# Kernel optimization log

Measured on AMD Instinct MI355X. Metric: run time of the kernel, lower is better.

## Reference

```python
import jax, jax.numpy as jnp
import numpy as np

HDIM = 1024
N_CLASSES = 50257
CUTOFFS = [2000, 10000, N_CLASSES]  # shortlist=2000, clusters: [2000,10000), [10000,50257)
DIV = 4.0
HEAD_SIZE = CUTOFFS[0] + 2  # shortlist + 2 cluster logits


def setup_inputs() -> dict:
    key = jax.random.key(0)
    ks = jax.random.split(key, 12)
    B, S, K = 8, 512, 256
    N = B * K
    hsz0 = int(HDIM // (DIV ** 1))  # 256
    hsz1 = int(HDIM // (DIV ** 2))  # 64
    osz0 = CUTOFFS[1] - CUTOFFS[0]  # 8000
    osz1 = CUTOFFS[2] - CUTOFFS[1]  # 40257
    w = 0.02
    return {
        "targets": jax.random.randint(ks[0], (N,), 0, N_CLASSES),
        "last_hidden_states": jax.random.normal(ks[1], (B, S, HDIM), dtype=jnp.float32),
        "cls_tokens_batch": jax.random.normal(ks[2], (B, HDIM), dtype=jnp.float32),
        "idx": jax.random.randint(ks[3], (B, K), 0, S),
        "head_W": jax.random.normal(ks[4], (HEAD_SIZE, HDIM), dtype=jnp.float32) * w,
        "head_b": jnp.zeros((HEAD_SIZE,), dtype=jnp.float32),
        "proj0_W": jax.random.normal(ks[5], (hsz0, HDIM), dtype=jnp.float32) * w,
        "out0_W": jax.random.normal(ks[6], (osz0, hsz0), dtype=jnp.float32) * w,
        "proj1_W": jax.random.normal(ks[7], (hsz1, HDIM), dtype=jnp.float32) * w,
        "out1_W": jax.random.normal(ks[8], (osz1, hsz1), dtype=jnp.float32) * w,
    }


def reference(targets, last_hidden_states, cls_tokens_batch, idx,
              head_W, head_b, proj0_W, out0_W, proj1_W, out1_W):
    # Gather context token embeddings: [B, K, H] -> [N, H]
    B, S, H = last_hidden_states.shape
    x = last_hidden_states[jnp.arange(B)[:, None], idx].reshape(-1, H)
    N = x.shape[0]
    c0, c1 = CUTOFFS[0], CUTOFFS[1]

    # Head: shortlist logits + per-cluster routing logits, [N, c0+2]
    head_logprob = jax.nn.log_softmax(x @ head_W.T + head_b, axis=-1)
    # Tail clusters: low-rank projection then output GEMM + log-softmax
    lp0 = jax.nn.log_softmax((x @ proj0_W.T) @ out0_W.T, axis=-1)  # [N, 8000]
    lp1 = jax.nn.log_softmax((x @ proj1_W.T) @ out1_W.T, axis=-1)  # [N, 40257]

    n = jnp.arange(N)
    t = targets
    short = head_logprob[n, jnp.clip(t, 0, c0 - 1)]
    mid = head_logprob[:, c0] + lp0[n, jnp.clip(t - c0, 0, lp0.shape[1] - 1)]
    high = head_logprob[:, c0 + 1] + lp1[n, jnp.clip(t - c1, 0, lp1.shape[1] - 1)]
    out = jnp.where(t < c0, short, jnp.where(t < c1, mid, high))  # target log-probs [N]
    loss = -jnp.mean(out)
    return out, loss
```

## Files before the change

kernel.cpp:

```cpp
#include <hip/hip_runtime.h>
#include <hip/hip_bf16.h>

#define NROWS 2048
#define L2E 1.4426950408889634f

typedef float f32x4 __attribute__((ext_vector_type(4)));
typedef __bf16 bf16x8 __attribute__((ext_vector_type(8)));
typedef short s16x8 __attribute__((ext_vector_type(8)));

typedef const __attribute__((address_space(1))) unsigned int* gas_t;
typedef __attribute__((address_space(3))) unsigned int* las_t;

__device__ __forceinline__ unsigned short f2bf(float f) {
    unsigned int u = __float_as_uint(f);
    unsigned int r = (u + 0x7FFFu + ((u >> 16) & 1u)) >> 16;
    return (unsigned short)r;
}
__device__ __forceinline__ float bf2f(unsigned short u) {
    return __uint_as_float((unsigned int)u << 16);
}
__device__ __forceinline__ f32x4 mfma16(s16x8 a, s16x8 b, f32x4 c) {
    return __builtin_amdgcn_mfma_f32_16x16x32_bf16(
        __builtin_bit_cast(bf16x8, a), __builtin_bit_cast(bf16x8, b), c, 0, 0, 0);
}

__global__ void k_prologue(const float* __restrict__ lhs, const int* __restrict__ idx,
                           const float* __restrict__ hw, const float* __restrict__ p0w,
                           const float* __restrict__ p1w, const float* __restrict__ hb,
                           const int* __restrict__ tgt,
                           unsigned short* __restrict__ xb, unsigned short* __restrict__ hWb,
                           unsigned short* __restrict__ pW01,
                           float* __restrict__ bias_s, int* __restrict__ tc,
                           unsigned long long* __restrict__ lossacc,
                           unsigned int* __restrict__ ticket) {
    int bid = blockIdx.x;
    if (bid < 2048) {
        int tid = bid * 256 + threadIdx.x;
        int n = tid >> 8;
        int c = (tid & 255) << 2;
        int b = n >> 8, k = n & 255;
        int srow = idx[(b << 8) + k];
        const float4 v = *reinterpret_cast<const float4*>(
            lhs + (((size_t)b << 9) + srow) * 1024 + c);
        ushort4 o = make_ushort4(f2bf(v.x), f2bf(v.y), f2bf(v.z), f2bf(v.w));
        *reinterpret_cast<ushort4*>(xb + (size_t)n * 1024 + c) = o;
        return;
    }
    bid -= 2048;
    if (bid < 2432) {
        long e = ((long)bid * 256 + threadIdx.x) * 4;
        const long B0 = 2048L * 1024;
        if (e < B0) {
            float4 v = *reinterpret_cast<const float4*>(hw + e);
            long row = e >> 10;
            ushort4 o;
            if (row < 2002) {
                o = make_ushort4(f2bf(v.x * L2E), f2bf(v.y * L2E), f2bf(v.z * L2E), f2bf(v.w * L2E));
            } else {
                o = make_ushort4(0, 0, 0, 0);
            }
            *reinterpret_cast<ushort4*>(hWb + e) = o;
        } else {
            long l = e - B0;
            long row = l >> 10;
            ushort4 o;
            if (row < 256) {
                float4 v = *reinterpret_cast<const float4*>(p0w + l);
                o = make_ushort4(f2bf(v.x), f2bf(v.y), f2bf(v.z), f2bf(v.w));
            } else if (row < 320) {
                float4 v = *reinterpret_cast<const float4*>(p1w + (l - 256L * 1024));
                o = make_ushort4(f2bf(v.x), f2bf(v.y), f2bf(v.z), f2bf(v.w));
            } else {
                o = make_ushort4(0, 0, 0, 0);
            }
            *reinterpret_cast<ushort4*>(pW01 + l) = o;
        }
        return;
    }
    bid -= 2432;
    int n = bid * 256 + threadIdx.x;
    if (n >= 2048) return;
    if (n == 0) { *lossacc = 0ull; *ticket = 0u; }
    bias_s[n] = (n < 2002) ? hb[n] * L2E : -1e30f;
    int t = tgt[n];
    tc[n] = min(t, 1999);
    tc[2048 + n] = min(max(t - 2000, 0), 7999);
    tc[4096 + n] = min(max(t - 10000, 0), 40256);
}

#define CVT_Y0 19
template <int NT>
__global__ __launch_bounds__(256)
void k_mid(const unsigned short* __restrict__ A, int lda,
           const unsigned short* __restrict__ B, int ldb,
           const float* __restrict__ bias, float* __restrict__ partial,
           unsigned short* __restrict__ hout, int hstride, int hcols, int fsplit,
           const float* __restrict__ o0w, const float* __restrict__ o1w,
           unsigned short* __restrict__ o0Wb, unsigned short* __restrict__ o1Wb) {
    if ((int)blockIdx.y >= CVT_Y0) {
        const long E0 = 8064L * 256;
        const long E1 = E0 + 40320L * 64;
        long cb = (long)(blockIdx.y - CVT_Y0) * 32 + blockIdx.x;
        long e = (cb * 256 + threadIdx.x) * 4;
        if (e >= E1) return;
        const float* src; unsigned short* dst; long rows; int colshift;
        if (e < E0) { src = o0w; dst = o0Wb; rows = 8000;  colshift = 8; }
        else        { e -= E0; src = o1w; dst = o1Wb; rows = 40257; colshift = 6; }
        long row = e >> colshift;
        ushort4 o;
        if (row < rows) {
            float4 v = *reinterpret_cast<const float4*>(src + e);
            o = make_ushort4(f2bf(v.x * L2E), f2bf(v.y * L2E), f2bf(v.z * L2E), f2bf(v.w * L2E));
        } else {
            o = make_ushort4(0, 0, 0, 0);
        }
        *reinterpret_cast<ushort4*>(dst + e) = o;
        return;
    }
    __shared__ unsigned short As[2][64 * 64];
    __shared__ unsigned short Bs[2][128 * 64];
    const int tid = threadIdx.x;
    const int lane = tid & 63, wid = tid >> 6;
    const int wc = wid;
    const int g = lane >> 4, cl = lane & 15;
    const int row0 = blockIdx.x * 64;
    const int col0 = blockIdx.y * 128;

    const int sr = wid * 8 + (lane >> 3);
    const int swz = ((lane & 7) ^ (lane >> 3)) * 8;
    const unsigned short* Ab = A + (size_t)(row0 + sr) * lda + swz;
    const unsigned short* Bb = B + (size_t)(col0 + sr) * ldb + swz;

    auto stage = [&](int buf, int kt) {
        unsigned short* la = &As[buf][wid * 8 * 64];
        unsigned short* lb = &Bs[buf][wid * 8 * 64];
#pragma unroll
        for (int i = 0; i < 2; ++i)
            __builtin_amdgcn_global_load_lds((gas_t)(const void*)(Ab + kt + (size_t)i * 32 * lda),
                                             (las_t)(void*)(la + i * 32 * 64), 16, 0, 0);
#pragma unroll
        for (int i = 0; i < 4; ++i)
            __builtin_amdgcn_global_load_lds((gas_t)(const void*)(Bb + kt + (size_t)i * 32 * ldb),
                                             (las_t)(void*)(lb + i * 32 * 64), 16, 0, 0);
    };

    f32x4 acc[4][2] = {};
    stage(0, 0);
    asm volatile("s_waitcnt vmcnt(0)" ::: "memory");
    __builtin_amdgcn_s_barrier();
    const int sA = (cl & 7);
    for (int t = 0; t < NT; ++t) {
        if (t + 1 < NT) stage((t + 1) & 1, (t + 1) * 64);
        const unsigned short* Al = &As[t & 1][cl * 64];
        const unsigned short* Bl = &Bs[t & 1][(wc * 32 + cl) * 64];
#pragma unroll
        for (int kk2 = 0; kk2 < 2; ++kk2) {
            const int slot = ((kk2 * 4 + g) ^ sA) * 8;
            s16x8 a[4], b[2];
#pragma unroll
            for (int mi = 0; mi < 4; ++mi)
                a[mi] = *reinterpret_cast<const s16x8*>(Al + mi * 16 * 64 + slot);
#pragma unroll
            for (int ni = 0; ni < 2; ++ni)
                b[ni] = *reinterpret_cast<const s16x8*>(Bl + ni * 16 * 64 + slot);
#pragma unroll
            for (int mi = 0; mi < 4; ++mi)
#pragma unroll
                for (int ni = 0; ni < 2; ++ni)
                    acc[mi][ni] = mfma16(a[mi], b[ni], acc[mi][ni]);
        }
        if (t + 1 < NT) {
            asm volatile("s_waitcnt vmcnt(0)" ::: "memory");
            __builtin_amdgcn_s_barrier();
        }
    }

    if ((int)blockIdx.y >= fsplit) {
        int c0 = col0 - fsplit * 128;
#pragma unroll
        for (int mi = 0; mi < 4; ++mi)
#pragma unroll
            for (int ni = 0; ni < 2; ++ni) {
                int col = c0 + wc * 32 + ni * 16 + cl;
                if (col < hcols) {
#pragma unroll
                    for (int r = 0; r < 4; ++r) {
                        int row = row0 + mi * 16 + g * 4 + r;
                        hout[(size_t)row * hstride + col] = f2bf(acc[mi][ni][r]);
                    }
                }
            }
    } else {
        float bv0 = bias[col0 + wc * 32 + cl];
        float bv1 = bias[col0 + wc * 32 + 16 + cl];
        int strip = blockIdx.y * 4 + wc;
#pragma unroll
        for (int mi = 0; mi < 4; ++mi)
#pragma unroll
            for (int r = 0; r < 4; ++r) {
                float s = __builtin_amdgcn_exp2f(acc[mi][0][r] + bv0)
                        + __builtin_amdgcn_exp2f(acc[mi][1][r] + bv1);
                s += __shfl_xor(s, 1, 64);
                s += __shfl_xor(s, 2, 64);
                s += __shfl_xor(s, 4, 64);
                s += __shfl_xor(s, 8, 64);
                if (cl == 0)
                    partial[(size_t)strip * NROWS + row0 + mi * 16 + g * 4 + r] = s;
            }
    }
}

#define OUT1_IT 5
__global__ __launch_bounds__(256, 3)
void k_tail(const unsigned short* __restrict__ h01, const unsigned short* __restrict__ o0Wb,
            const unsigned short* __restrict__ o1Wb, const unsigned short* __restrict__ xb,
            const float* __restrict__ headW, const float* __restrict__ hb,
            const float* __restrict__ o0w, const float* __restrict__ o1w,
            const int* __restrict__ tc,
            float* __restrict__ p0, float* __restrict__ p1,
            float* __restrict__ tgh, float* __restrict__ r0, float* __restrict__ r1,
            float* __restrict__ tg0, float* __restrict__ tg1) {
    __shared__ unsigned short smemB[2][128 * 64];
    __shared__ unsigned short smemA[2][64 * 64];
    const int tid = threadIdx.x;
    const int lane = tid & 63, wid = tid >> 6;
    const int g = lane >> 4, cl = lane & 15;
    int bid = blockIdx.x;

    if (bid < 1008) {
        const int wr = wid >> 1, wc = wid & 1;
        const int row0 = (bid & 15) * 128 + wr * 64;
        const int yb = bid >> 4;
        const int t0 = yb * OUT1_IT;
        s16x8 a[4][2];
#pragma unroll
        for (int mi = 0; mi < 4; ++mi)
#pragma unroll
            for (int kk = 0; kk < 2; ++kk)
                a[mi][kk] = *reinterpret_cast<const s16x8*>(
                    h01 + (size_t)(row0 + mi * 16 + cl) * 320 + 256 + kk * 32 + g * 8);
        const int sr = wid * 8 + (lane >> 3);
        const int swz = ((lane & 7) ^ (lane >> 3)) * 8;
        auto stage = [&](int buf, int tile) {
            const unsigned short* gb = o1Wb + ((size_t)tile * 128 + sr) * 64 + swz;
            unsigned short* lb = &smemB[buf][wid * 8 * 64];
#pragma unroll
            for (int i = 0; i < 4; ++i)
                __builtin_amdgcn_global_load_lds((gas_t)(const void*)(gb + (size_t)i * 32 * 64),
                                                 (las_t)(void*)(lb + i * 32 * 64), 16, 0, 0);
        };
        float sexp[4][4] = {};
        const f32x4 z4 = {0.f, 0.f, 0.f, 0.f};
        stage(0, t0);
        asm volatile("s_waitcnt vmcnt(0)" ::: "memory");
        __builtin_amdgcn_s_barrier();
        int buf = 0;
        const int sA = (cl & 7);
#pragma unroll 1
        for (int it = 0; it < OUT1_IT; ++it) {
            if (it + 1 < OUT1_IT) stage(buf ^ 1, t0 + it + 1);
            const unsigned short* Bl = smemB[buf];
#pragma unroll
            for (int ni = 0; ni < 4; ++ni) {
                const unsigned short* br = Bl + (wc * 64 + ni * 16 + cl) * 64;
                s16x8 b0 = *reinterpret_cast<const s16x8*>(br + (g ^ sA) * 8);
                s16x8 b1 = *reinterpret_cast<const s16x8*>(br + ((4 + g) ^ sA) * 8);
                f32x4 acc[4];
#pragma unroll
                for (int mi = 0; mi < 4; ++mi)
                    acc[mi] = mfma16(a[mi][0], b0, z4);
#pragma unroll
                for (int mi = 0; mi < 4; ++mi)
                    acc[mi] = mfma16(a[mi][1], b1, acc[mi]);
#pragma unroll
                for (int mi = 0; mi < 4; ++mi)
#pragma unroll
                    for (int r = 0; r < 4; ++r)
                        sexp[mi][r] += __builtin_amdgcn_exp2f(acc[mi][r]);
            }
            if (it + 1 < OUT1_IT) {
                asm volatile("s_waitcnt vmcnt(0)" ::: "memory");
                __builtin_amdgcn_s_barrier();
                buf ^= 1;
            }
        }
#pragma unroll
        for (int mi = 0; mi < 4; ++mi)
#pragma unroll
            for (int r = 0; r < 4; ++r) {
                float s = sexp[mi][r];
                s += __shfl_xor(s, 1, 64);
                s += __shfl_xor(s, 2, 64);
                s += __shfl_xor(s, 4, 64);
                s += __shfl_xor(s, 8, 64);
                if (cl == 0)
                    p1[(size_t)(yb * 2 + wc) * NROWS + row0 + mi * 16 + g * 4 + r] = s;
            }
        return;
    }
    if (bid < 3024) {
        int b = bid - 1008;
        const int row0 = (b & 31) * 64;
        const int col0 = (b >> 5) * 128;
        const int sr = wid * 8 + (lane >> 3);
        const int swz = ((lane & 7) ^ (lane >> 3)) * 8;
        const unsigned short* Ab = h01 + (size_t)(row0 + sr) * 320 + swz;
        const unsigned short* Bb = o0Wb + (size_t)(col0 + sr) * 256 + swz;
        auto stage = [&](int buf, int kt) {
            unsigned short* la = &smemA[buf][wid * 8 * 64];
            unsigned short* lb = &smemB[buf][wid * 8 * 64];
#pragma unroll
            for (int i = 0; i < 2; ++i)
                __builtin_amdgcn_global_load_lds((gas_t)(const void*)(Ab + kt + (size_t)i * 32 * 320),
                                                 (las_t)(void*)(la + i * 32 * 64), 16, 0, 0);
#pragma unroll
            for (int i = 0; i < 4; ++i)
                __builtin_amdgcn_global_load_lds((gas_t)(const void*)(Bb + kt + (size_t)i * 32 * 256),
                                                 (las_t)(void*)(lb + i * 32 * 64), 16, 0, 0);
        };
        f32x4 acc[4][2] = {};
        stage(0, 0);
        asm volatile("s_waitcnt vmcnt(0)" ::: "memory");
        __builtin_amdgcn_s_barrier();
        const int sA = (cl & 7);
        for (int t = 0; t < 4; ++t) {
            if (t < 3) stage((t + 1) & 1, (t + 1) * 64);
            const unsigned short* Al = &smemA[t & 1][cl * 64];
            const unsigned short* Bl = &smemB[t & 1][(wid * 32 + cl) * 64];
#pragma unroll
            for (int kk2 = 0; kk2 < 2; ++kk2) {
                const int slot = ((kk2 * 4 + g) ^ sA) * 8;
                s16x8 a[4], bb[2];
#pragma unroll
                for (int mi = 0; mi < 4; ++mi)
                    a[mi] = *reinterpret_cast<const s16x8*>(Al + mi * 16 * 64 + slot);
#pragma unroll
                for (int ni = 0; ni < 2; ++ni)
                    bb[ni] = *reinterpret_cast<const s16x8*>(Bl + ni * 16 * 64 + slot);
#pragma unroll
                for (int mi = 0; mi < 4; ++mi)
#pragma unroll
                    for (int ni = 0; ni < 2; ++ni)
                        acc[mi][ni] = mfma16(a[mi], bb[ni], acc[mi][ni]);
            }
            if (t < 3) {
                asm volatile("s_waitcnt vmcnt(0)" ::: "memory");
                __builtin_amdgcn_s_barrier();
            }
        }
        int strip = (b >> 5) * 4 + wid;
#pragma unroll
        for (int mi = 0; mi < 4; ++mi)
#pragma unroll
            for (int r = 0; r < 4; ++r) {
                float s = __builtin_amdgcn_exp2f(acc[mi][0][r])
                        + __builtin_amdgcn_exp2f(acc[mi][1][r]);
                s += __shfl_xor(s, 1, 64);
                s += __shfl_xor(s, 2, 64);
                s += __shfl_xor(s, 4, 64);
                s += __shfl_xor(s, 8, 64);
                if (cl == 0)
                    p0[(size_t)strip * NROWS + row0 + mi * 16 + g * 4 + r] = s;
            }
        return;
    }
    int b = bid - 3024;
    int n = (b * 256 + tid) >> 6;
    int tch = tc[n], tc0 = tc[2048 + n], tc1 = tc[4096 + n];
    const unsigned short* xr = xb + (size_t)n * 1024 + lane * 16;
    s16x8 x0 = *reinterpret_cast<const s16x8*>(xr);
    s16x8 x1 = *reinterpret_cast<const s16x8*>(xr + 8);
    const float* wh = headW + (size_t)tch * 1024 + lane * 16;
    const float* wa = headW + (size_t)2000 * 1024 + lane * 16;
    const float* wb = headW + (size_t)2001 * 1024 + lane * 16;
    float dh = 0.f, da = 0.f, db = 0.f;
#pragma unroll
    for (int i = 0; i < 8; ++i) {
        float xv = bf2f((unsigned short)x0[i]);
        dh += xv * wh[i]; da += xv * wa[i]; db += xv * wb[i];
    }
#pragma unroll
    for (int i = 0; i < 8; ++i) {
        float xv = bf2f((unsigned short)x1[i]);
        dh += xv * wh[8 + i]; da += xv * wa[8 + i]; db += xv * wb[8 + i];
    }
    ushort4 h0v = *reinterpret_cast<const ushort4*>(h01 + (size_t)n * 320 + lane * 4);
    float4 w0v = *reinterpret_cast<const float4*>(o0w + (size_t)tc0 * 256 + lane * 4);
    float d2 = bf2f(h0v.x) * w0v.x + bf2f(h0v.y) * w0v.y +
               bf2f(h0v.z) * w0v.z + bf2f(h0v.w) * w0v.w;
    float d3 = bf2f(h01[(size_t)n * 320 + 256 + lane]) * o1w[(size_t)tc1 * 64 + lane];
#pragma unroll
    for (int m = 1; m < 64; m <<= 1) {
        dh += __shfl_xor(dh, m, 64);
        da += __shfl_xor(da, m, 64);
        db += __shfl_xor(db, m, 64);
        d2 += __shfl_xor(d2, m, 64);
        d3 += __shfl_xor(d3, m, 64);
    }
    if (lane == 0) {
        tgh[n] = dh + hb[tch];
        r0[n] = da + hb[2000];
        r1[n] = db + hb[2001];
        tg0[n] = d2;
        tg1[n] = d3;
    }
}

__global__ void k_finalize(const float* __restrict__ ph, const float* __restrict__ p0,
                           const float* __restrict__ p1, const float* __restrict__ tgh,
                           const float* __restrict__ r0, const float* __restrict__ r1,
                           const float* __restrict__ tg0, const float* __restrict__ tg1,
                           const int* __restrict__ tgt, float* __restrict__ outv,
                           unsigned long long* __restrict__ lossacc,
                           unsigned int* __restrict__ ticket) {
    const int tid = threadIdx.x;
    const int l4 = tid & 3;
    const int n = blockIdx.x * 64 + (tid >> 2);
    float sh = 0.f, s0 = 0.f, s1 = 0.f;
    for (int s = l4; s < 64; s += 4)  sh += ph[(size_t)s * NROWS + n];
    for (int s = l4; s < 252; s += 4) s0 += p0[(size_t)s * NROWS + n];
    for (int s = l4; s < 126; s += 4) s1 += p1[(size_t)s * NROWS + n];
    sh += __shfl_xor(sh, 1, 64); sh += __shfl_xor(sh, 2, 64);
    s0 += __shfl_xor(s0, 1, 64); s0 += __shfl_xor(s0, 2, 64);
    s1 += __shfl_xor(s1, 1, 64); s1 += __shfl_xor(s1, 2, 64);
    s0 -= 64.f;
    s1 -= 63.f;
    float lh = __logf(sh);
    int t = tgt[n];
    float o;
    if (t < 2000) o = tgh[n] - lh;
    else if (t < 10000) o = (r0[n] - lh) + (tg0[n] - __logf(s0));
    else o = (r1[n] - lh) + (tg1[n] - __logf(s1));
    __shared__ float red[64];
    if (l4 == 0) { outv[n] = o; red[tid >> 2] = o; }
    __syncthreads();
    for (int s2 = 32; s2 > 0; s2 >>= 1) {
        if (tid < s2) red[tid] += red[tid + s2];
        __syncthreads();
    }
    if (tid == 0) {
        long long fx = __double2ll_rn((double)red[0] * 1048576.0);
        atomicAdd(lossacc, (unsigned long long)fx);
        __threadfence();
        unsigned int tk = atomicAdd(ticket, 1u);
        if (tk == 31u) {
            unsigned long long v = atomicAdd(lossacc, 0ull);
            outv[NROWS] = (float)(-((double)(long long)v / 1048576.0) / 2048.0);
        }
    }
}

extern "C" void kernel_launch(void* const* d_in, const int* in_sizes, int n_in,
                              void* d_out, int out_size, void* d_ws, size_t ws_size,
                              hipStream_t stream) {
    const int* targets   = (const int*)d_in[0];
    const float* lhs     = (const float*)d_in[1];
    const int* idx       = (const int*)d_in[3];
    const float* head_W  = (const float*)d_in[4];
    const float* head_b  = (const float*)d_in[5];
    const float* proj0_W = (const float*)d_in[6];
    const float* out0_W  = (const float*)d_in[7];
    const float* proj1_W = (const float*)d_in[8];
    const float* out1_W  = (const float*)d_in[9];

    char* ws = (char*)d_ws;
    size_t off = 0;
    auto alloc = [&](size_t bytes) -> void* {
        void* p = ws + off;
        off += (bytes + 255) & ~(size_t)255;
        return p;
    };

    unsigned short* xb   = (unsigned short*)alloc((size_t)2048 * 1024 * 2);
    unsigned short* wB   = (unsigned short*)alloc((size_t)2432 * 1024 * 2);
    unsigned short* hWb  = wB;
    unsigned short* pW01 = wB + (size_t)2048 * 1024;
    unsigned short* o0Wb = (unsigned short*)alloc((size_t)8064 * 256 * 2);
    unsigned short* o1Wb = (unsigned short*)alloc((size_t)40320 * 64 * 2);
    unsigned short* h01  = (unsigned short*)alloc((size_t)2048 * 320 * 2);
    float* ph  = (float*)alloc((size_t)64 * 2048 * 4);
    float* p0  = (float*)alloc((size_t)252 * 2048 * 4);
    float* p1  = (float*)alloc((size_t)126 * 2048 * 4);
    float* tgh = (float*)alloc(2048 * 4);
    float* r0  = (float*)alloc(2048 * 4);
    float* r1  = (float*)alloc(2048 * 4);
    float* tg0 = (float*)alloc(2048 * 4);
    float* tg1 = (float*)alloc(2048 * 4);
    int*   tc  = (int*)alloc(3 * 2048 * 4);
    float* bias_s = (float*)alloc(2048 * 4);
    unsigned long long* lossacc = (unsigned long long*)alloc(8);
    unsigned int* ticket = (unsigned int*)alloc(4);

    k_prologue<<<4488, 256, 0, stream>>>(lhs, idx, head_W, proj0_W, proj1_W,
                                         head_b, targets,
                                         xb, hWb, pW01, bias_s, tc, lossacc, ticket);

    k_mid<16><<<dim3(32, CVT_Y0 + 142), 256, 0, stream>>>(
        xb, 1024, wB, 1024, bias_s, ph, h01, 320, 320, 16,
        out0_W, out1_W, o0Wb, o1Wb);

    k_tail<<<3536, 256, 0, stream>>>(h01, o0Wb, o1Wb, xb, head_W, head_b,
                                     out0_W, out1_W, tc,
                                     p0, p1, tgh, r0, r1, tg0, tg1);

    float* outv = (float*)d_out;
    k_finalize<<<32, 256, 0, stream>>>(ph, p0, p1, tgh, r0, r1, tg0, tg1, targets,
                                       outv, lossacc, ticket);
}
```

Measured before the change: 107.0 us.

## Move out-weight bf16 conversion into prologue and remap tail block order

Moves the fp32-to-bf16 conversion of out0_W and out1_W out of the mid GEMM kernel and into the prologue, so k_mm launches only the 19 GEMM tile rows. k_tail block indices are remapped with a stride-8 permutation across its three sections, likely to spread blocks across XCDs for better cache locality. The trade-off is that the conversion no longer overlaps with the head/projection GEMM and instead lengthens the memory-bound prologue.

```diff
diff --git a/kernel.cpp b/kernel.cpp
--- a/kernel.cpp
+++ b/kernel.cpp
@@ -26,10 +26,12 @@
 
 __global__ void k_prologue(const float* __restrict__ lhs, const int* __restrict__ idx,
                            const float* __restrict__ hw, const float* __restrict__ p0w,
-                           const float* __restrict__ p1w, const float* __restrict__ hb,
+                           const float* __restrict__ p1w, const float* __restrict__ o0w,
+                           const float* __restrict__ o1w, const float* __restrict__ hb,
                            const int* __restrict__ tgt,
                            unsigned short* __restrict__ xb, unsigned short* __restrict__ hWb,
-                           unsigned short* __restrict__ pW01,
+                           unsigned short* __restrict__ pW01, unsigned short* __restrict__ o0Wb,
+                           unsigned short* __restrict__ o1Wb,
                            float* __restrict__ bias_s, int* __restrict__ tc,
                            unsigned long long* __restrict__ lossacc,
                            unsigned int* __restrict__ ticket) {
@@ -47,22 +49,20 @@
         return;
     }
     bid -= 2048;
-    if (bid < 2432) {
+    if (bid < 6968) {
+        const long B0 = 2048L * 1024;
+        const long B1 = B0 + 384L * 1024;
+        const long B2 = B1 + 8064L * 256;
+        const long B3 = B2 + 40320L * 64;
         long e = ((long)bid * 256 + threadIdx.x) * 4;
-        const long B0 = 2048L * 1024;
-        if (e < B0) {
-            float4 v = *reinterpret_cast<const float4*>(hw + e);
-            long row = e >> 10;
-            ushort4 o;
-            if (row < 2002) {
-                o = make_ushort4(f2bf(v.x * L2E), f2bf(v.y * L2E), f2bf(v.z * L2E), f2bf(v.w * L2E));
-            } else {
-                o = make_ushort4(0, 0, 0, 0);
-            }
-            *reinterpret_cast<ushort4*>(hWb + e) = o;
-        } else {
+        if (e >= B3) return;
+        const float* src; unsigned short* dst; long rows; int colshift; long base;
+        float sc;
+        if (e < B0)      { base = 0;  src = hw;  dst = hWb;  rows = 2002;  colshift = 10; sc = L2E; }
+        else if (e < B1) {
             long l = e - B0;
             long row = l >> 10;
+            unsigned short* d = pW01 + l;
             ushort4 o;
             if (row < 256) {
                 float4 v = *reinterpret_cast<const float4*>(p0w + l);
@@ -73,11 +73,24 @@
             } else {
                 o = make_ushort4(0, 0, 0, 0);
             }
-            *reinterpret_cast<ushort4*>(pW01 + l) = o;
-        }
+            *reinterpret_cast<ushort4*>(d) = o;
+            return;
+        }
+        else if (e < B2) { base = B1; src = o0w; dst = o0Wb; rows = 8000;  colshift = 8; sc = L2E; }
+        else             { base = B2; src = o1w; dst = o1Wb; rows = 40257; colshift = 6; sc = L2E; }
+        long l = e - base;
+        long row = l >> colshift;
+        ushort4 o;
+        if (row < rows) {
+            float4 v = *reinterpret_cast<const float4*>(src + l);
+            o = make_ushort4(f2bf(v.x * sc), f2bf(v.y * sc), f2bf(v.z * sc), f2bf(v.w * sc));
+        } else {
+            o = make_ushort4(0, 0, 0, 0);
+        }
+        *reinterpret_cast<ushort4*>(dst + l) = o;
         return;
     }
-    bid -= 2432;
+    bid -= 6968;
     int n = bid * 256 + threadIdx.x;
     if (n >= 2048) return;
     if (n == 0) { *lossacc = 0ull; *ticket = 0u; }
@@ -88,35 +101,12 @@
     tc[4096 + n] = min(max(t - 10000, 0), 40256);
 }
 
-#define CVT_Y0 19
 template <int NT>
 __global__ __launch_bounds__(256)
-void k_mid(const unsigned short* __restrict__ A, int lda,
-           const unsigned short* __restrict__ B, int ldb,
-           const float* __restrict__ bias, float* __restrict__ partial,
-           unsigned short* __restrict__ hout, int hstride, int hcols, int fsplit,
-           const float* __restrict__ o0w, const float* __restrict__ o1w,
-           unsigned short* __restrict__ o0Wb, unsigned short* __restrict__ o1Wb) {
-    if ((int)blockIdx.y >= CVT_Y0) {
-        const long E0 = 8064L * 256;
-        const long E1 = E0 + 40320L * 64;
-        long cb = (long)(blockIdx.y - CVT_Y0) * 32 + blockIdx.x;
-        long e = (cb * 256 + threadIdx.x) * 4;
-        if (e >= E1) return;
-        const float* src; unsigned short* dst; long rows; int colshift;
-        if (e < E0) { src = o0w; dst = o0Wb; rows = 8000;  colshift = 8; }
-        else        { e -= E0; src = o1w; dst = o1Wb; rows = 40257; colshift = 6; }
-        long row = e >> colshift;
-        ushort4 o;
-        if (row < rows) {
-            float4 v = *reinterpret_cast<const float4*>(src + e);
-            o = make_ushort4(f2bf(v.x * L2E), f2bf(v.y * L2E), f2bf(v.z * L2E), f2bf(v.w * L2E));
-        } else {
-            o = make_ushort4(0, 0, 0, 0);
-        }
-        *reinterpret_cast<ushort4*>(dst + e) = o;
-        return;
-    }
+void k_mm(const unsigned short* __restrict__ A, int lda,
+          const unsigned short* __restrict__ B, int ldb,
+          const float* __restrict__ bias, float* __restrict__ partial,
+          unsigned short* __restrict__ hout, int hstride, int hcols, int fsplit) {
     __shared__ unsigned short As[2][64 * 64];
     __shared__ unsigned short Bs[2][128 * 64];
     const int tid = threadIdx.x;
@@ -225,9 +215,10 @@
     const int tid = threadIdx.x;
     const int lane = tid & 63, wid = tid >> 6;
     const int g = lane >> 4, cl = lane & 15;
-    int bid = blockIdx.x;
-
-    if (bid < 1008) {
+    int raw = (int)blockIdx.x;
+
+    if (raw < 1008) {
+        int bid = (raw & 7) * 126 + (raw >> 3);
         const int wr = wid >> 1, wc = wid & 1;
         const int row0 = (bid & 15) * 128 + wr * 64;
         const int yb = bid >> 4;
@@ -298,8 +289,9 @@
             }
         return;
     }
-    if (bid < 3024) {
-        int b = bid - 1008;
+    if (raw < 3024) {
+        int b2 = raw - 1008;
+        int b = (b2 & 7) * 252 + (b2 >> 3);
         const int row0 = (b & 31) * 64;
         const int col0 = (b >> 5) * 128;
         const int sr = wid * 8 + (lane >> 3);
@@ -364,8 +356,9 @@
             }
         return;
     }
-    int b = bid - 3024;
-    int n = (b * 256 + tid) >> 6;
+    int b3 = raw - 3024;
+    int bid = (b3 & 7) * 64 + (b3 >> 3);
+    int n = (bid * 256 + tid) >> 6;
     int tch = tc[n], tc0 = tc[2048 + n], tc1 = tc[4096 + n];
     const unsigned short* xr = xb + (size_t)n * 1024 + lane * 16;
     s16x8 x0 = *reinterpret_cast<const s16x8*>(xr);
@@ -491,17 +484,16 @@
     unsigned long long* lossacc = (unsigned long long*)alloc(8);
     unsigned int* ticket = (unsigned int*)alloc(4);
 
-    k_prologue<<<4488, 256, 0, stream>>>(lhs, idx, head_W, proj0_W, proj1_W,
+    k_prologue<<<9024, 256, 0, stream>>>(lhs, idx, head_W, proj0_W, proj1_W, out0_W, out1_W,
                                          head_b, targets,
-                                         xb, hWb, pW01, bias_s, tc, lossacc, ticket);
-
-    k_mid<16><<<dim3(32, CVT_Y0 + 142), 256, 0, stream>>>(
-        xb, 1024, wB, 1024, bias_s, ph, h01, 320, 320, 16,
-        out0_W, out1_W, o0Wb, o1Wb);
-
-    k_tail<<<3536, 256, 0, stream>>>(h01, o0Wb, o1Wb, xb, head_W, head_b,
-                                     out0_W, out1_W, tc,
-                                     p0, p1, tgh, r0, r1, tg0, tg1);
+                                         xb, hWb, pW01, o0Wb, o1Wb, bias_s, tc,
+                                         lossacc, ticket);
+
+    k_mm<16><<<dim3(32, 19), 256, 0, stream>>>(
+        xb, 1024, wB, 1024, bias_s, ph, h01, 320, 320, 16);
+
+    k_tail<<<3536, 256, 0, stream>>>(h01, o0Wb, o1Wb, xb, head_W, head_b, out0_W, out1_W,
+                                     tc, p0, p1, tgh, r0, r1, tg0, tg1);
 
     float* outv = (float*)d_out;
     k_finalize<<<32, 256, 0, stream>>>(ph, p0, p1, tgh, r0, r1, tg0, tg1, targets,
```

New measurement: 109.7 us. 1.02x slower.
